# Kernel optimization log

Measured on AMD Instinct MI355X. Metric: run time of the kernel, lower is better.

Reference implementation:

```python
import jax, jax.numpy as jnp
import numpy as np

N1 = 4096
N2 = 4096


def _encoder(x, w1, b1, w2, b2, w3, b3):
    # fc1 -> fc2 -> fc3 -> relu (relu only after fc3, matching the torch code)
    h = x @ w1.T + b1
    h = h @ w2.T + b2
    h = h @ w3.T + b3
    return jax.nn.relu(h)


def _self_attention(x, adj, alpha, W):
    # tmp_i = sum_j [adj_ij==1] * alpha_ij * W * x_j ; tmp_i /= deg_i ; tmp_i += x_i (only if deg_i != 0)
    a = (adj == 1).astype(x.dtype)          # [N, N]
    deg = a.sum(axis=1)                     # [N]
    agg = (a * alpha) @ x                   # [N, 64] masked weighted aggregation
    agg = agg * W[0, 0]
    safe_deg = jnp.maximum(deg, 1.0)
    out = agg / safe_deg[:, None] + x       # residual
    return jnp.where((deg != 0.0)[:, None], out, jnp.zeros_like(out))


def setup_inputs() -> dict:
    key = jax.random.key(0)
    ks = jax.random.split(key, 20)
    s = 0.02  # weight scale to keep activations sane through the 4096->256->128->64 MLP
    inp = {
        "x1": jax.random.normal(ks[0], (N1, N1), jnp.float32),
        "x2": jax.random.normal(ks[1], (N2, N2), jnp.float32),
        "adj1": jax.random.randint(ks[2], (N1, N1), 0, 2, jnp.int32),
        "adj2": jax.random.randint(ks[3], (N2, N2), 0, 2, jnp.int32),
        "e1_w1": jax.random.normal(ks[4], (256, N1), jnp.float32) * s,
        "e1_b1": jnp.zeros((256,), jnp.float32),
        "e1_w2": jax.random.normal(ks[5], (128, 256), jnp.float32) * s,
        "e1_b2": jnp.zeros((128,), jnp.float32),
        "e1_w3": jax.random.normal(ks[6], (64, 128), jnp.float32) * s,
        "e1_b3": jnp.zeros((64,), jnp.float32),
        "e2_w1": jax.random.normal(ks[7], (256, N2), jnp.float32) * s,
        "e2_b1": jnp.zeros((256,), jnp.float32),
        "e2_w2": jax.random.normal(ks[8], (128, 256), jnp.float32) * s,
        "e2_b2": jnp.zeros((128,), jnp.float32),
        "e2_w3": jax.random.normal(ks[9], (64, 128), jnp.float32) * s,
        "e2_b3": jnp.zeros((64,), jnp.float32),
        "W": jax.random.normal(ks[10], (1, 1), jnp.float32),
        "alpha1": jax.random.normal(ks[11], (N1, N1), jnp.float32),
        "clf_w": jax.random.normal(ks[12], (2, (N1 + N2) * 64), jnp.float32) * s,
        "clf_b": jnp.zeros((2,), jnp.float32),
    }
    return inp


def reference(x1, x2, adj1, adj2,
              e1_w1, e1_b1, e1_w2, e1_b2, e1_w3, e1_b3,
              e2_w1, e2_b1, e2_w2, e2_b2, e2_w3, e2_b3,
              W, alpha1, clf_w, clf_b):
    h1 = _encoder(x1, e1_w1, e1_b1, e1_w2, e1_b2, e1_w3, e1_b3)  # [N1, 64]
    h2 = _encoder(x2, e2_w1, e2_b1, e2_w2, e2_b2, e2_w3, e2_b3)  # [N2, 64]
    # NOTE: original torch code uses self.alpha1 for BOTH graphs (alpha2 is unused)
    new1 = _self_attention(h1, adj1, alpha1, W)
    new2 = _self_attention(h2, adj2, alpha1[:N2, :N2], W)
    feat = jnp.concatenate([new1, new2], axis=0).reshape(1, -1)  # [1, (N1+N2)*64]
    return feat @ clf_w.T + clf_b  # [1, 2]
```

## Files before the change

kernel.cpp:

```cpp
#include <hip/hip_runtime.h>
#include <hip/hip_bf16.h>
#include <stdint.h>

#define N 4096

typedef __attribute__((ext_vector_type(4))) float f32x4;
typedef __attribute__((ext_vector_type(8))) short s16x8;

__device__ inline unsigned short f2bf(float f) {
    unsigned int u = __float_as_uint(f);
    u += 0x7fffu + ((u >> 16) & 1u);
    return (unsigned short)(u >> 16);
}
__device__ inline float bf2f(unsigned short h) {
    return __uint_as_float(((unsigned int)h) << 16);
}

__global__ void k0a(const float* __restrict__ w2a, const float* __restrict__ w3a,
                    const float* __restrict__ b1a, const float* __restrict__ b2a, const float* __restrict__ b3a,
                    const float* __restrict__ w2b, const float* __restrict__ w3b,
                    const float* __restrict__ b1b, const float* __restrict__ b2b, const float* __restrict__ b3b,
                    float* __restrict__ T, float* __restrict__ beff) {
    const int g  = blockIdx.x >> 5;
    const int nb = blockIdx.x & 31;
    const float* w2 = g ? w2b : w2a;
    const float* w3 = g ? w3b : w3a;
    const int c  = threadIdx.x;
    const int n0 = nb * 2;
    float a0 = 0.f, a1 = 0.f;
#pragma unroll 4
    for (int r = 0; r < 128; ++r) {
        float w = w2[r * 256 + c];
        a0 += w3[n0 * 128 + r] * w;
        a1 += w3[n0 * 128 + 128 + r] * w;
    }
    float* Tg = T + g * 64 * 256;
    Tg[n0 * 256 + c]       = a0;
    Tg[(n0 + 1) * 256 + c] = a1;

    if (nb == 0) {
        __shared__ float u[128];
        const float* b1 = g ? b1b : b1a;
        const float* b2 = g ? b2b : b2a;
        const float* b3 = g ? b3b : b3a;
        if (threadIdx.x < 128) {
            int r = threadIdx.x;
            float s = 0.f;
            for (int cc = 0; cc < 256; ++cc) s += w2[r * 256 + cc] * b1[cc];
            u[r] = s + b2[r];
        }
        __syncthreads();
        if (threadIdx.x < 64) {
            int n = threadIdx.x;
            float s = 0.f;
            for (int r = 0; r < 128; ++r) s += w3[n * 128 + r] * u[r];
            beff[g * 64 + n] = s + b3[n];
        }
    }
}

__global__ void k0b(const float* __restrict__ w1a, const float* __restrict__ w1b,
                    const float* __restrict__ T,
                    unsigned short* __restrict__ Whi, unsigned short* __restrict__ Wlo) {
    const int b  = blockIdx.x;
    const int g  = b >> 7, n8 = (b >> 4) & 7, kc = b & 15;
    const float* w1 = g ? w1b : w1a;
    const float* Tg = T + (g * 64 + n8 * 8) * 256;
    const int kx = kc * 256 + threadIdx.x;
    float acc[8] = {0, 0, 0, 0, 0, 0, 0, 0};
    for (int r = 0; r < 256; ++r) {
        float w = w1[r * N + kx];
#pragma unroll
        for (int j = 0; j < 8; ++j) acc[j] += Tg[j * 256 + r] * w;
    }
#pragma unroll
    for (int j = 0; j < 8; ++j) {
        size_t idx = (size_t)(g * 64 + n8 * 8 + j) * N + kx;
        unsigned short hi = f2bf(acc[j]);
        Whi[idx] = hi;
        Wlo[idx] = f2bf(acc[j] - bf2f(hi));
    }
}

__global__ __launch_bounds__(256) void k1(const float* __restrict__ x1, const float* __restrict__ x2,
                                          const unsigned short* __restrict__ Whi,
                                          const unsigned short* __restrict__ Wlo,
                                          const float* __restrict__ beff,
                                          float* __restrict__ hf, unsigned short* __restrict__ hT) {
    const int b  = blockIdx.x;
    const int g  = b & 1;
    const int i0 = (b >> 1) * 16;
    const float* x = g ? x2 : x1;
    const size_t goff = (size_t)g * 64 * N;

    __shared__ unsigned short Ah[16 * 72], Al[16 * 72];
    __shared__ unsigned short Bh[64 * 72], Bl[64 * 72];

    const int t = threadIdx.x;
    const int lane = t & 63, w = t >> 6;
    const int arow = t >> 4, ac4 = (t & 15) * 4;
    const int brow = (t * 16) >> 7, bkh = ((t * 16) & 127) >> 1;
    const int q = lane >> 4, l15 = lane & 15;

    f32x4 acc = {0.f, 0.f, 0.f, 0.f};

    for (int kk = 0; kk < 64; ++kk) {
        const int k0 = kk * 64;
        float4 av  = *(const float4*)&x[(size_t)(i0 + arow) * N + k0 + ac4];
        uint4  bh0 = *(const uint4*)&Whi[goff + (size_t)brow * N + k0 + bkh];
        uint4  bh1 = *(const uint4*)&Whi[goff + (size_t)(brow + 32) * N + k0 + bkh];
        uint4  bl0 = *(const uint4*)&Wlo[goff + (size_t)brow * N + k0 + bkh];
        uint4  bl1 = *(const uint4*)&Wlo[goff + (size_t)(brow + 32) * N + k0 + bkh];
        __syncthreads();
        unsigned short hx = f2bf(av.x), hy = f2bf(av.y), hz = f2bf(av.z), hw = f2bf(av.w);
        unsigned short lx = f2bf(av.x - bf2f(hx)), ly = f2bf(av.y - bf2f(hy));
        unsigned short lz = f2bf(av.z - bf2f(hz)), lw = f2bf(av.w - bf2f(hw));
        *(uint2*)&Ah[arow * 72 + ac4] = make_uint2((unsigned)hx | ((unsigned)hy << 16),
                                                   (unsigned)hz | ((unsigned)hw << 16));
        *(uint2*)&Al[arow * 72 + ac4] = make_uint2((unsigned)lx | ((unsigned)ly << 16),
                                                   (unsigned)lz | ((unsigned)lw << 16));
        *(uint4*)&Bh[brow * 72 + bkh] = bh0;
        *(uint4*)&Bh[(brow + 32) * 72 + bkh] = bh1;
        *(uint4*)&Bl[brow * 72 + bkh] = bl0;
        *(uint4*)&Bl[(brow + 32) * 72 + bkh] = bl1;
        __syncthreads();
#pragma unroll
        for (int c = 0; c < 2; ++c) {
            const int kf = c * 32 + q * 8;
            s16x8 ah = *(const s16x8*)&Ah[l15 * 72 + kf];
            s16x8 al = *(const s16x8*)&Al[l15 * 72 + kf];
            s16x8 bh = *(const s16x8*)&Bh[(w * 16 + l15) * 72 + kf];
            s16x8 bl = *(const s16x8*)&Bl[(w * 16 + l15) * 72 + kf];
            acc = __builtin_amdgcn_mfma_f32_16x16x32_bf16(al, bh, acc, 0, 0, 0);
            acc = __builtin_amdgcn_mfma_f32_16x16x32_bf16(ah, bl, acc, 0, 0, 0);
            acc = __builtin_amdgcn_mfma_f32_16x16x32_bf16(ah, bh, acc, 0, 0, 0);
        }
    }

    const int n = w * 16 + l15;
    const float be = beff[g * 64 + n];
    unsigned short pk[4];
#pragma unroll
    for (int r = 0; r < 4; ++r) {
        int i = i0 + q * 4 + r;
        float v = acc[r] + be;
        v = fmaxf(v, 0.f);
        hf[(size_t)(g * N + i) * 64 + n] = v;
        pk[r] = f2bf(v);
    }
    *(ushort4*)&hT[(size_t)(g * 64 + n) * N + i0 + q * 4] = make_ushort4(pk[0], pk[1], pk[2], pk[3]);
}

__global__ __launch_bounds__(256) void k2(const int* __restrict__ adj1, const int* __restrict__ adj2,
                                          const float* __restrict__ alpha, const float* __restrict__ Wp,
                                          const unsigned short* __restrict__ hT, const float* __restrict__ hf,
                                          float* __restrict__ outv) {
    const int i0 = blockIdx.x * 16;
    __shared__ unsigned short A1s[16 * 72], A2s[16 * 72];
    __shared__ unsigned short B1s[64 * 72], B2s[64 * 72];
    __shared__ float degred[2 * 256];
    __shared__ float degs[2 * 16];

    const int t = threadIdx.x;
    const int lane = t & 63, w = t >> 6;
    const int arow = t >> 4, ac4 = (t & 15) * 4;
    const int brow = (t * 16) >> 7, bkh = ((t * 16) & 127) >> 1;
    const int q = lane >> 4, l15 = lane & 15;

    f32x4 acc1 = {0.f, 0.f, 0.f, 0.f}, acc2 = {0.f, 0.f, 0.f, 0.f};
    int deg1 = 0, deg2 = 0;

    for (int kk = 0; kk < 64; ++kk) {
        const int k0 = kk * 64;
        const size_t aidx = (size_t)(i0 + arow) * N + k0 + ac4;
        float4 al = *(const float4*)&alpha[aidx];
        int4 j1 = *(const int4*)&adj1[aidx];
        int4 j2 = *(const int4*)&adj2[aidx];
        uint4 b10 = *(const uint4*)&hT[(size_t)brow * N + k0 + bkh];
        uint4 b11 = *(const uint4*)&hT[(size_t)(brow + 32) * N + k0 + bkh];
        uint4 b20 = *(const uint4*)&hT[(size_t)(64 + brow) * N + k0 + bkh];
        uint4 b21 = *(const uint4*)&hT[(size_t)(64 + brow + 32) * N + k0 + bkh];
        unsigned short bx = f2bf(al.x), by = f2bf(al.y), bz = f2bf(al.z), bw = f2bf(al.w);
        __syncthreads();
        unsigned int lo1 = (j1.x == 1 ? (unsigned int)bx : 0u) | ((j1.y == 1 ? (unsigned int)by : 0u) << 16);
        unsigned int hi1 = (j1.z == 1 ? (unsigned int)bz : 0u) | ((j1.w == 1 ? (unsigned int)bw : 0u) << 16);
        unsigned int lo2 = (j2.x == 1 ? (unsigned int)bx : 0u) | ((j2.y == 1 ? (unsigned int)by : 0u) << 16);
        unsigned int hi2 = (j2.z == 1 ? (unsigned int)bz : 0u) | ((j2.w == 1 ? (unsigned int)bw : 0u) << 16);
        deg1 += (j1.x == 1) + (j1.y == 1) + (j1.z == 1) + (j1.w == 1);
        deg2 += (j2.x == 1) + (j2.y == 1) + (j2.z == 1) + (j2.w == 1);
        *(uint2*)&A1s[arow * 72 + ac4] = make_uint2(lo1, hi1);
        *(uint2*)&A2s[arow * 72 + ac4] = make_uint2(lo2, hi2);
        *(uint4*)&B1s[brow * 72 + bkh] = b10;
        *(uint4*)&B1s[(brow + 32) * 72 + bkh] = b11;
        *(uint4*)&B2s[brow * 72 + bkh] = b20;
        *(uint4*)&B2s[(brow + 32) * 72 + bkh] = b21;
        __syncthreads();
#pragma unroll
        for (int c = 0; c < 2; ++c) {
            const int kf = c * 32 + q * 8;
            s16x8 a1f = *(const s16x8*)&A1s[l15 * 72 + kf];
            s16x8 b1f = *(const s16x8*)&B1s[(w * 16 + l15) * 72 + kf];
            acc1 = __builtin_amdgcn_mfma_f32_16x16x32_bf16(a1f, b1f, acc1, 0, 0, 0);
            s16x8 a2f = *(const s16x8*)&A2s[l15 * 72 + kf];
            s16x8 b2f = *(const s16x8*)&B2s[(w * 16 + l15) * 72 + kf];
            acc2 = __builtin_amdgcn_mfma_f32_16x16x32_bf16(a2f, b2f, acc2, 0, 0, 0);
        }
    }

    degred[t]       = (float)deg1;
    degred[256 + t] = (float)deg2;
    __syncthreads();
    if (t < 32) {
        int g = t >> 4, r = t & 15;
        float s = 0.f;
        for (int j = 0; j < 16; ++j) s += degred[g * 256 + r * 16 + j];
        degs[g * 16 + r] = s;
    }
    __syncthreads();

    const float W00 = Wp[0];
    const int n = w * 16 + l15;
#pragma unroll
    for (int r = 0; r < 4; ++r) {
        int iloc = q * 4 + r;
        int i = i0 + iloc;
        float dg1 = degs[iloc];
        float hv1 = hf[(size_t)i * 64 + n];
        float v1 = (dg1 != 0.f) ? (acc1[r] * W00 / fmaxf(dg1, 1.f) + hv1) : 0.f;
        outv[(size_t)i * 64 + n] = v1;
        float dg2 = degs[16 + iloc];
        float hv2 = hf[(size_t)(N + i) * 64 + n];
        float v2 = (dg2 != 0.f) ? (acc2[r] * W00 / fmaxf(dg2, 1.f) + hv2) : 0.f;
        outv[(size_t)(N + i) * 64 + n] = v2;
    }
}

__global__ __launch_bounds__(256) void k3a(const float* __restrict__ feat, const float* __restrict__ clfw,
                                           float* __restrict__ part) {
    const int t = threadIdx.x;
    const size_t idx = (size_t)blockIdx.x * 2048 + (size_t)t * 8;
    float4 a0 = *(const float4*)&feat[idx];
    float4 a1 = *(const float4*)&feat[idx + 4];
    float4 c0 = *(const float4*)&clfw[idx];
    float4 c1 = *(const float4*)&clfw[idx + 4];
    float4 d0 = *(const float4*)&clfw[524288 + idx];
    float4 d1 = *(const float4*)&clfw[524288 + idx + 4];
    float s0 = a0.x * c0.x + a0.y * c0.y + a0.z * c0.z + a0.w * c0.w
             + a1.x * c1.x + a1.y * c1.y + a1.z * c1.z + a1.w * c1.w;
    float s1 = a0.x * d0.x + a0.y * d0.y + a0.z * d0.z + a0.w * d0.w
             + a1.x * d1.x + a1.y * d1.y + a1.z * d1.z + a1.w * d1.w;
    __shared__ float r0[256], r1[256];
    r0[t] = s0; r1[t] = s1;
    __syncthreads();
    for (int s = 128; s > 0; s >>= 1) {
        if (t < s) { r0[t] += r0[t + s]; r1[t] += r1[t + s]; }
        __syncthreads();
    }
    if (t == 0) { part[blockIdx.x * 2] = r0[0]; part[blockIdx.x * 2 + 1] = r1[0]; }
}

__global__ void k3b(const float* __restrict__ part, const float* __restrict__ clfb,
                    float* __restrict__ outp) {
    const int t = threadIdx.x;
    __shared__ float r0[256], r1[256];
    r0[t] = part[t * 2]; r1[t] = part[t * 2 + 1];
    __syncthreads();
    for (int s = 128; s > 0; s >>= 1) {
        if (t < s) { r0[t] += r0[t + s]; r1[t] += r1[t + s]; }
        __syncthreads();
    }
    if (t == 0) { outp[0] = r0[0] + clfb[0]; outp[1] = r1[0] + clfb[1]; }
}

extern "C" void kernel_launch(void* const* d_in, const int* in_sizes, int n_in,
                              void* d_out, int out_size, void* d_ws, size_t ws_size,
                              hipStream_t stream) {
    const float* x1   = (const float*)d_in[0];
    const float* x2   = (const float*)d_in[1];
    const int*   adj1 = (const int*)d_in[2];
    const int*   adj2 = (const int*)d_in[3];
    const float* e1w1 = (const float*)d_in[4];
    const float* e1b1 = (const float*)d_in[5];
    const float* e1w2 = (const float*)d_in[6];
    const float* e1b2 = (const float*)d_in[7];
    const float* e1w3 = (const float*)d_in[8];
    const float* e1b3 = (const float*)d_in[9];
    const float* e2w1 = (const float*)d_in[10];
    const float* e2b1 = (const float*)d_in[11];
    const float* e2w2 = (const float*)d_in[12];
    const float* e2b2 = (const float*)d_in[13];
    const float* e2w3 = (const float*)d_in[14];
    const float* e2b3 = (const float*)d_in[15];
    const float* Wp   = (const float*)d_in[16];
    const float* alph = (const float*)d_in[17];
    const float* clfw = (const float*)d_in[18];
    const float* clfb = (const float*)d_in[19];

    char* wsb = (char*)d_ws;
    unsigned short* Whi = (unsigned short*)(wsb);
    unsigned short* Wlo = (unsigned short*)(wsb + (1u << 20));
    float* newv = (float*)(wsb);
    unsigned short* hT  = (unsigned short*)(wsb + (2u << 20));
    float* hf   = (float*)(wsb + (3u << 20));
    float* T    = (float*)(wsb + (5u << 20));
    float* beff = (float*)(wsb + (5u << 20) + (1u << 17));
    float* part = (float*)(wsb + (5u << 20) + (1u << 17) + 4096);

    hipLaunchKernelGGL(k0a, dim3(64), dim3(256), 0, stream,
                       e1w2, e1w3, e1b1, e1b2, e1b3, e2w2, e2w3, e2b1, e2b2, e2b3, T, beff);
    hipLaunchKernelGGL(k0b, dim3(256), dim3(256), 0, stream, e1w1, e2w1, T, Whi, Wlo);
    hipLaunchKernelGGL(k1, dim3(512), dim3(256), 0, stream, x1, x2, Whi, Wlo, beff, hf, hT);
    hipLaunchKernelGGL(k2, dim3(256), dim3(256), 0, stream, adj1, adj2, alph, Wp, hT, hf, newv);
    hipLaunchKernelGGL(k3a, dim3(256), dim3(256), 0, stream, newv, clfw, part);
    hipLaunchKernelGGL(k3b, dim3(1), dim3(256), 0, stream, part, clfb, (float*)d_out);
}
```

Baseline: 448.3 us.

## Split K across waves with direct-to-register MFMA loads in k1 and k2

k1 and k2 no longer stage operands through shared memory with two barriers per K step. Each of the four waves now handles a quarter of K and computes all 64 output columns, loading A and B fragments straight from global memory into registers. Partial accumulators are reduced through shared memory once at the end. This removes per-iteration barriers and LDS traffic but raises register use, makes global loads less coalesced (16-byte strided rows), and adds a final reduction. Unroll pragmas are also tuned in the small precompute kernels.

```diff
diff --git a/kernel.cpp b/kernel.cpp
--- a/kernel.cpp
+++ b/kernel.cpp
@@ -28,7 +28,7 @@
     const int c  = threadIdx.x;
     const int n0 = nb * 2;
     float a0 = 0.f, a1 = 0.f;
-#pragma unroll 4
+#pragma unroll 8
     for (int r = 0; r < 128; ++r) {
         float w = w2[r * 256 + c];
         a0 += w3[n0 * 128 + r] * w;
@@ -68,6 +68,7 @@
     const float* Tg = T + (g * 64 + n8 * 8) * 256;
     const int kx = kc * 256 + threadIdx.x;
     float acc[8] = {0, 0, 0, 0, 0, 0, 0, 0};
+#pragma unroll 8
     for (int r = 0; r < 256; ++r) {
         float w = w1[r * N + kx];
 #pragma unroll
@@ -93,59 +94,61 @@
     const float* x = g ? x2 : x1;
     const size_t goff = (size_t)g * 64 * N;
 
-    __shared__ unsigned short Ah[16 * 72], Al[16 * 72];
-    __shared__ unsigned short Bh[64 * 72], Bl[64 * 72];
-
     const int t = threadIdx.x;
-    const int lane = t & 63, w = t >> 6;
-    const int arow = t >> 4, ac4 = (t & 15) * 4;
-    const int brow = (t * 16) >> 7, bkh = ((t * 16) & 127) >> 1;
+    const int lane = t & 63, kg = t >> 6;
     const int q = lane >> 4, l15 = lane & 15;
 
-    f32x4 acc = {0.f, 0.f, 0.f, 0.f};
-
-    for (int kk = 0; kk < 64; ++kk) {
-        const int k0 = kk * 64;
-        float4 av  = *(const float4*)&x[(size_t)(i0 + arow) * N + k0 + ac4];
-        uint4  bh0 = *(const uint4*)&Whi[goff + (size_t)brow * N + k0 + bkh];
-        uint4  bh1 = *(const uint4*)&Whi[goff + (size_t)(brow + 32) * N + k0 + bkh];
-        uint4  bl0 = *(const uint4*)&Wlo[goff + (size_t)brow * N + k0 + bkh];
-        uint4  bl1 = *(const uint4*)&Wlo[goff + (size_t)(brow + 32) * N + k0 + bkh];
-        __syncthreads();
-        unsigned short hx = f2bf(av.x), hy = f2bf(av.y), hz = f2bf(av.z), hw = f2bf(av.w);
-        unsigned short lx = f2bf(av.x - bf2f(hx)), ly = f2bf(av.y - bf2f(hy));
-        unsigned short lz = f2bf(av.z - bf2f(hz)), lw = f2bf(av.w - bf2f(hw));
-        *(uint2*)&Ah[arow * 72 + ac4] = make_uint2((unsigned)hx | ((unsigned)hy << 16),
-                                                   (unsigned)hz | ((unsigned)hw << 16));
-        *(uint2*)&Al[arow * 72 + ac4] = make_uint2((unsigned)lx | ((unsigned)ly << 16),
-                                                   (unsigned)lz | ((unsigned)lw << 16));
-        *(uint4*)&Bh[brow * 72 + bkh] = bh0;
-        *(uint4*)&Bh[(brow + 32) * 72 + bkh] = bh1;
-        *(uint4*)&Bl[brow * 72 + bkh] = bl0;
-        *(uint4*)&Bl[(brow + 32) * 72 + bkh] = bl1;
-        __syncthreads();
+    __shared__ float accs[4][4][64][4];
+
+    f32x4 acc[4];
+#pragma unroll
+    for (int ng = 0; ng < 4; ++ng) acc[ng] = (f32x4){0.f, 0.f, 0.f, 0.f};
+
+    const float* xrow = x + (size_t)(i0 + l15) * N;
+    for (int kk = 0; kk < 16; ++kk) {
 #pragma unroll
         for (int c = 0; c < 2; ++c) {
-            const int kf = c * 32 + q * 8;
-            s16x8 ah = *(const s16x8*)&Ah[l15 * 72 + kf];
-            s16x8 al = *(const s16x8*)&Al[l15 * 72 + kf];
-            s16x8 bh = *(const s16x8*)&Bh[(w * 16 + l15) * 72 + kf];
-            s16x8 bl = *(const s16x8*)&Bl[(w * 16 + l15) * 72 + kf];
-            acc = __builtin_amdgcn_mfma_f32_16x16x32_bf16(al, bh, acc, 0, 0, 0);
-            acc = __builtin_amdgcn_mfma_f32_16x16x32_bf16(ah, bl, acc, 0, 0, 0);
-            acc = __builtin_amdgcn_mfma_f32_16x16x32_bf16(ah, bh, acc, 0, 0, 0);
+            const int ka = kg * 1024 + kk * 64 + c * 32 + q * 8;
+            float4 a0 = *(const float4*)&xrow[ka];
+            float4 a1 = *(const float4*)&xrow[ka + 4];
+            s16x8 bh[4], bl[4];
+#pragma unroll
+            for (int ng = 0; ng < 4; ++ng) {
+                const size_t bo = goff + (size_t)(ng * 16 + l15) * N + ka;
+                bh[ng] = *(const s16x8*)&Whi[bo];
+                bl[ng] = *(const s16x8*)&Wlo[bo];
+            }
+            float xv[8] = {a0.x, a0.y, a0.z, a0.w, a1.x, a1.y, a1.z, a1.w};
+            s16x8 ah, al;
+#pragma unroll
+            for (int j = 0; j < 8; ++j) {
+                unsigned short h = f2bf(xv[j]);
+                ah[j] = (short)h;
+                al[j] = (short)f2bf(xv[j] - bf2f(h));
+            }
+#pragma unroll
+            for (int ng = 0; ng < 4; ++ng) {
+                acc[ng] = __builtin_amdgcn_mfma_f32_16x16x32_bf16(al, bh[ng], acc[ng], 0, 0, 0);
+                acc[ng] = __builtin_amdgcn_mfma_f32_16x16x32_bf16(ah, bl[ng], acc[ng], 0, 0, 0);
+                acc[ng] = __builtin_amdgcn_mfma_f32_16x16x32_bf16(ah, bh[ng], acc[ng], 0, 0, 0);
+            }
         }
     }
-
-    const int n = w * 16 + l15;
+#pragma unroll
+    for (int ng = 0; ng < 4; ++ng)
+#pragma unroll
+        for (int r = 0; r < 4; ++r) accs[kg][ng][lane][r] = acc[ng][r];
+    __syncthreads();
+
+    const int n = kg * 16 + l15;
     const float be = beff[g * 64 + n];
     unsigned short pk[4];
 #pragma unroll
     for (int r = 0; r < 4; ++r) {
-        int i = i0 + q * 4 + r;
-        float v = acc[r] + be;
+        float v = accs[0][kg][lane][r] + accs[1][kg][lane][r]
+                + accs[2][kg][lane][r] + accs[3][kg][lane][r] + be;
         v = fmaxf(v, 0.f);
-        hf[(size_t)(g * N + i) * 64 + n] = v;
+        hf[(size_t)(g * N + i0 + q * 4 + r) * 64 + n] = v;
         pk[r] = f2bf(v);
     }
     *(ushort4*)&hT[(size_t)(g * 64 + n) * N + i0 + q * 4] = make_ushort4(pk[0], pk[1], pk[2], pk[3]);
@@ -156,82 +159,97 @@
                                           const unsigned short* __restrict__ hT, const float* __restrict__ hf,
                                           float* __restrict__ outv) {
     const int i0 = blockIdx.x * 16;
-    __shared__ unsigned short A1s[16 * 72], A2s[16 * 72];
-    __shared__ unsigned short B1s[64 * 72], B2s[64 * 72];
-    __shared__ float degred[2 * 256];
-    __shared__ float degs[2 * 16];
-
     const int t = threadIdx.x;
-    const int lane = t & 63, w = t >> 6;
-    const int arow = t >> 4, ac4 = (t & 15) * 4;
-    const int brow = (t * 16) >> 7, bkh = ((t * 16) & 127) >> 1;
+    const int lane = t & 63, kg = t >> 6;
     const int q = lane >> 4, l15 = lane & 15;
 
-    f32x4 acc1 = {0.f, 0.f, 0.f, 0.f}, acc2 = {0.f, 0.f, 0.f, 0.f};
+    __shared__ float accs[4][4][64][8];
+    __shared__ float degp[4][64][2];
+    __shared__ float degf[2][16];
+
+    f32x4 acc[4][2];
+#pragma unroll
+    for (int ng = 0; ng < 4; ++ng) {
+        acc[ng][0] = (f32x4){0.f, 0.f, 0.f, 0.f};
+        acc[ng][1] = (f32x4){0.f, 0.f, 0.f, 0.f};
+    }
     int deg1 = 0, deg2 = 0;
 
-    for (int kk = 0; kk < 64; ++kk) {
-        const int k0 = kk * 64;
-        const size_t aidx = (size_t)(i0 + arow) * N + k0 + ac4;
-        float4 al = *(const float4*)&alpha[aidx];
-        int4 j1 = *(const int4*)&adj1[aidx];
-        int4 j2 = *(const int4*)&adj2[aidx];
-        uint4 b10 = *(const uint4*)&hT[(size_t)brow * N + k0 + bkh];
-        uint4 b11 = *(const uint4*)&hT[(size_t)(brow + 32) * N + k0 + bkh];
-        uint4 b20 = *(const uint4*)&hT[(size_t)(64 + brow) * N + k0 + bkh];
-        uint4 b21 = *(const uint4*)&hT[(size_t)(64 + brow + 32) * N + k0 + bkh];
-        unsigned short bx = f2bf(al.x), by = f2bf(al.y), bz = f2bf(al.z), bw = f2bf(al.w);
-        __syncthreads();
-        unsigned int lo1 = (j1.x == 1 ? (unsigned int)bx : 0u) | ((j1.y == 1 ? (unsigned int)by : 0u) << 16);
-        unsigned int hi1 = (j1.z == 1 ? (unsigned int)bz : 0u) | ((j1.w == 1 ? (unsigned int)bw : 0u) << 16);
-        unsigned int lo2 = (j2.x == 1 ? (unsigned int)bx : 0u) | ((j2.y == 1 ? (unsigned int)by : 0u) << 16);
-        unsigned int hi2 = (j2.z == 1 ? (unsigned int)bz : 0u) | ((j2.w == 1 ? (unsigned int)bw : 0u) << 16);
-        deg1 += (j1.x == 1) + (j1.y == 1) + (j1.z == 1) + (j1.w == 1);
-        deg2 += (j2.x == 1) + (j2.y == 1) + (j2.z == 1) + (j2.w == 1);
-        *(uint2*)&A1s[arow * 72 + ac4] = make_uint2(lo1, hi1);
-        *(uint2*)&A2s[arow * 72 + ac4] = make_uint2(lo2, hi2);
-        *(uint4*)&B1s[brow * 72 + bkh] = b10;
-        *(uint4*)&B1s[(brow + 32) * 72 + bkh] = b11;
-        *(uint4*)&B2s[brow * 72 + bkh] = b20;
-        *(uint4*)&B2s[(brow + 32) * 72 + bkh] = b21;
-        __syncthreads();
+    const size_t rowoff = (size_t)(i0 + l15) * N;
+    for (int kk = 0; kk < 16; ++kk) {
 #pragma unroll
         for (int c = 0; c < 2; ++c) {
-            const int kf = c * 32 + q * 8;
-            s16x8 a1f = *(const s16x8*)&A1s[l15 * 72 + kf];
-            s16x8 b1f = *(const s16x8*)&B1s[(w * 16 + l15) * 72 + kf];
-            acc1 = __builtin_amdgcn_mfma_f32_16x16x32_bf16(a1f, b1f, acc1, 0, 0, 0);
-            s16x8 a2f = *(const s16x8*)&A2s[l15 * 72 + kf];
-            s16x8 b2f = *(const s16x8*)&B2s[(w * 16 + l15) * 72 + kf];
-            acc2 = __builtin_amdgcn_mfma_f32_16x16x32_bf16(a2f, b2f, acc2, 0, 0, 0);
+            const int ka = kg * 1024 + kk * 64 + c * 32 + q * 8;
+            const size_t ao = rowoff + ka;
+            float4 a0 = *(const float4*)&alpha[ao];
+            float4 a1 = *(const float4*)&alpha[ao + 4];
+            int4 j10 = *(const int4*)&adj1[ao];
+            int4 j11 = *(const int4*)&adj1[ao + 4];
+            int4 j20 = *(const int4*)&adj2[ao];
+            int4 j21 = *(const int4*)&adj2[ao + 4];
+            s16x8 b1[4], b2[4];
+#pragma unroll
+            for (int ng = 0; ng < 4; ++ng) {
+                const size_t bo = (size_t)(ng * 16 + l15) * N + ka;
+                b1[ng] = *(const s16x8*)&hT[bo];
+                b2[ng] = *(const s16x8*)&hT[(size_t)64 * N + bo];
+            }
+            float av[8] = {a0.x, a0.y, a0.z, a0.w, a1.x, a1.y, a1.z, a1.w};
+            int m1[8] = {j10.x == 1, j10.y == 1, j10.z == 1, j10.w == 1,
+                         j11.x == 1, j11.y == 1, j11.z == 1, j11.w == 1};
+            int m2[8] = {j20.x == 1, j20.y == 1, j20.z == 1, j20.w == 1,
+                         j21.x == 1, j21.y == 1, j21.z == 1, j21.w == 1};
+            s16x8 af1, af2;
+#pragma unroll
+            for (int j = 0; j < 8; ++j) {
+                short bv = (short)f2bf(av[j]);
+                af1[j] = m1[j] ? bv : (short)0;
+                af2[j] = m2[j] ? bv : (short)0;
+                deg1 += m1[j];
+                deg2 += m2[j];
+            }
+#pragma unroll
+            for (int ng = 0; ng < 4; ++ng) {
+                acc[ng][0] = __builtin_amdgcn_mfma_f32_16x16x32_bf16(af1, b1[ng], acc[ng][0], 0, 0, 0);
+                acc[ng][1] = __builtin_amdgcn_mfma_f32_16x16x32_bf16(af2, b2[ng], acc[ng][1], 0, 0, 0);
+            }
         }
     }
-
-    degred[t]       = (float)deg1;
-    degred[256 + t] = (float)deg2;
+#pragma unroll
+    for (int ng = 0; ng < 4; ++ng)
+#pragma unroll
+        for (int gg = 0; gg < 2; ++gg)
+#pragma unroll
+            for (int r = 0; r < 4; ++r) accs[kg][ng][lane][gg * 4 + r] = acc[ng][gg][r];
+    degp[kg][lane][0] = (float)deg1;
+    degp[kg][lane][1] = (float)deg2;
     __syncthreads();
     if (t < 32) {
-        int g = t >> 4, r = t & 15;
+        int gg = t >> 4, row = t & 15;
         float s = 0.f;
-        for (int j = 0; j < 16; ++j) s += degred[g * 256 + r * 16 + j];
-        degs[g * 16 + r] = s;
+#pragma unroll
+        for (int w = 0; w < 4; ++w)
+#pragma unroll
+            for (int qq = 0; qq < 4; ++qq) s += degp[w][qq * 16 + row][gg];
+        degf[gg][row] = s;
     }
     __syncthreads();
 
     const float W00 = Wp[0];
-    const int n = w * 16 + l15;
+    const int n = kg * 16 + l15;
 #pragma unroll
     for (int r = 0; r < 4; ++r) {
         int iloc = q * 4 + r;
         int i = i0 + iloc;
-        float dg1 = degs[iloc];
+        float s1 = accs[0][kg][lane][r] + accs[1][kg][lane][r]
+                 + accs[2][kg][lane][r] + accs[3][kg][lane][r];
+        float s2 = accs[0][kg][lane][4 + r] + accs[1][kg][lane][4 + r]
+                 + accs[2][kg][lane][4 + r] + accs[3][kg][lane][4 + r];
+        float dg1 = degf[0][iloc], dg2 = degf[1][iloc];
         float hv1 = hf[(size_t)i * 64 + n];
-        float v1 = (dg1 != 0.f) ? (acc1[r] * W00 / fmaxf(dg1, 1.f) + hv1) : 0.f;
-        outv[(size_t)i * 64 + n] = v1;
-        float dg2 = degs[16 + iloc];
+        outv[(size_t)i * 64 + n] = (dg1 != 0.f) ? (s1 * W00 / fmaxf(dg1, 1.f) + hv1) : 0.f;
         float hv2 = hf[(size_t)(N + i) * 64 + n];
-        float v2 = (dg2 != 0.f) ? (acc2[r] * W00 / fmaxf(dg2, 1.f) + hv2) : 0.f;
-        outv[(size_t)(N + i) * 64 + n] = v2;
+        outv[(size_t)(N + i) * 64 + n] = (dg2 != 0.f) ? (s2 * W00 / fmaxf(dg2, 1.f) + hv2) : 0.f;
     }
 }
 
```

After: 455.3 us. Within noise of the previous version (+1.6%).
